# Kernel optimization log

Measured on AMD Instinct MI355X. Metric: run time of the kernel, lower is better.

## Reference

```python
import jax, jax.numpy as jnp
import numpy as np

HEADS = 8

def setup_inputs() -> dict:
    key = jax.random.key(0)
    ks = jax.random.split(key, 6)
    N, C, L = 8, 512, 2048
    s = 0.02
    return {
        'x':  jax.random.normal(ks[0], (N, C, L), dtype=jnp.float32),
        'Wq': jax.random.normal(ks[1], (C, C), dtype=jnp.float32) * s,
        'Wk': jax.random.normal(ks[2], (C, C), dtype=jnp.float32) * s,
        'Wv': jax.random.normal(ks[3], (C, C), dtype=jnp.float32) * s,
        'Wo': jax.random.normal(ks[4], (C, C), dtype=jnp.float32) * s,
        'bo': jnp.zeros((C,), dtype=jnp.float32),
    }

def reference(x, Wq, Wk, Wv, Wo, bo):
    N, C, L = x.shape
    h = HEADS
    d = C // h
    scale = C ** (-0.5)  # note: scales by full channels, as in the original

    def proj(W):
        # Conv1d(k=1, bias=False) == per-position linear: [N,C,L] -> [N,L,h,d]
        y = jnp.einsum('oc,ncl->nlo', W, x)
        return y.reshape(N, L, h, d)

    q, k, v = proj(Wq), proj(Wk), proj(Wv)

    qk = jnp.einsum('nqhd,nkhd->nhqk', q, k)  # [N,h,L,L]
    causal_mask = jnp.tril(jnp.ones((L, L), dtype=bool))
    qk = jnp.where(causal_mask, qk, -jnp.inf)
    attn = jax.nn.softmax(qk * scale, axis=-1)

    out = jnp.einsum('nhqk,nkhd->nqhd', attn, v)  # [N,L,h,d]
    out = out.reshape(N, L, C).transpose(0, 2, 1)  # n (h d) l
    return jnp.einsum('oc,ncl->nol', Wo, out) + bo[None, :, None]
```

## Files before the change

kernel.cpp:

```cpp
#include <hip/hip_runtime.h>
#include <math.h>

typedef __bf16 bf16;
typedef __attribute__((ext_vector_type(8))) __bf16 bf16x8;
typedef __attribute__((ext_vector_type(4))) float f32x4;
typedef unsigned short u16;
typedef unsigned int u32;

constexpr int Nn = 8, Cc = 512, Ll = 2048, Hh = 8, Dd = 64;
constexpr float kScale = 0.044194173824159216f;
constexpr size_t NCL = (size_t)Nn * Cc * Ll;
constexpr size_t WSZ = (size_t)Cc * Cc;

static __device__ __forceinline__ u16 bfbits(bf16 v) {
    union { bf16 b; u16 u; } x; x.b = v; return x.u;
}

#define MFMA(a, b, c) __builtin_amdgcn_mfma_f32_16x16x32_bf16((a), (b), (c), 0, 0, 0)

static __device__ __forceinline__ void async16(const bf16* g, bf16* l) {
    __builtin_amdgcn_global_load_lds(
        (const __attribute__((address_space(1))) void*)g,
        (__attribute__((address_space(3))) void*)l, 16, 0, 0);
}

__global__ __launch_bounds__(256) void xpose_kernel(
    const float* __restrict__ x, bf16* __restrict__ xT)
{
    __shared__ bf16 Ts[64][72];
    const int lt = blockIdx.x, ct = blockIdx.y, n = blockIdx.z;
    const int tid = threadIdx.x;

    const int cr = tid >> 2, l0 = (tid & 3) * 16;
    const float* src = x + ((size_t)(n * Cc + ct * 64 + cr)) * Ll + lt * 64 + l0;
#pragma unroll
    for (int i = 0; i < 4; i++) {
        float4 v = *(const float4*)(src + i * 4);
        Ts[l0 + i * 4 + 0][cr] = (bf16)v.x;
        Ts[l0 + i * 4 + 1][cr] = (bf16)v.y;
        Ts[l0 + i * 4 + 2][cr] = (bf16)v.z;
        Ts[l0 + i * 4 + 3][cr] = (bf16)v.w;
    }
    __syncthreads();

    const int lr = tid >> 2, c0 = (tid & 3) * 16;
    bf16* dst = xT + ((size_t)(n * Ll + lt * 64 + lr)) * Cc + ct * 64 + c0;
    *(bf16x8*)(dst)     = *(const bf16x8*)&Ts[lr][c0];
    *(bf16x8*)(dst + 8) = *(const bf16x8*)&Ts[lr][c0 + 8];
}

__global__ __launch_bounds__(256) void cvtw_kernel(
    const float* __restrict__ Wq, const float* __restrict__ Wk,
    const float* __restrict__ Wv, const float* __restrict__ Wo,
    bf16* __restrict__ Wb)
{
    size_t i = (size_t)blockIdx.x * 256 + threadIdx.x;
    int w = (int)(i >> 16);
    size_t o = i & 65535;
    const float* src = (w == 0) ? Wq : (w == 1) ? Wk : (w == 2) ? Wv : Wo;
    float4 v = ((const float4*)src)[o];
    ushort4 u;
    u.x = bfbits((bf16)v.x); u.y = bfbits((bf16)v.y);
    u.z = bfbits((bf16)v.z); u.w = bfbits((bf16)v.w);
    *(ushort4*)(Wb + (size_t)w * WSZ + o * 4) = u;
}

__global__ __launch_bounds__(256) void qkv_gemm(
    const bf16* __restrict__ xT, const bf16* __restrict__ Wb,
    bf16* __restrict__ Qt, bf16* __restrict__ Kt, bf16* __restrict__ Vb)
{
    const int lt = blockIdx.x, ow = blockIdx.y, n = blockIdx.z;
    const int widx = ow >> 2, otile = ow & 3;

    __shared__ bf16 Xs[128 * 64];
    __shared__ bf16 Ws[128 * 64];

    const int tid = threadIdx.x;
    const int lane = tid & 63, wv = tid >> 6;
    const int m = lane & 15, quad = lane >> 4;
    const int rh = wv & 1, ch = wv >> 1;

    const bf16* __restrict__ W = Wb + (size_t)widx * WSZ + (size_t)otile * 128 * Cc;
    const bf16* __restrict__ X = xT + (size_t)(n * Ll + lt * 128) * Cc;

    int srow[4], scol[4];
#pragma unroll
    for (int i = 0; i < 4; i++) {
        int q = i * 256 + tid;
        srow[i] = q >> 3;
        scol[i] = ((q ^ (q >> 3)) & 7) * 8;
    }

    f32x4 acc[4][4] = {};

    for (int c0 = 0; c0 < Cc; c0 += 64) {
#pragma unroll
        for (int i = 0; i < 4; i++)
            async16(&X[(size_t)srow[i] * Cc + c0 + scol[i]], &Xs[(i * 256 + tid) * 8]);
#pragma unroll
        for (int i = 0; i < 4; i++)
            async16(&W[(size_t)srow[i] * Cc + c0 + scol[i]], &Ws[(i * 256 + tid) * 8]);
        __syncthreads();

        const bf16* TA = (widx < 2) ? Xs : Ws;
        const bf16* TB = (widx < 2) ? Ws : Xs;
#pragma unroll
        for (int kk = 0; kk < 2; kk++) {
            const int sw = (((kk * 4 + quad) ^ (m & 7)) * 8);
            bf16x8 af[4], bfr[4];
#pragma unroll
            for (int t = 0; t < 4; t++)
                af[t] = *(const bf16x8*)&TA[(rh * 64 + t * 16 + m) * 64 + sw];
#pragma unroll
            for (int u = 0; u < 4; u++)
                bfr[u] = *(const bf16x8*)&TB[(ch * 64 + u * 16 + m) * 64 + sw];
#pragma unroll
            for (int t = 0; t < 4; t++)
#pragma unroll
                for (int u = 0; u < 4; u++)
                    acc[t][u] = MFMA(af[t], bfr[u], acc[t][u]);
        }
        __syncthreads();
    }

    if (widx < 2) {
        bf16* __restrict__ OUT = (widx == 0) ? Qt : Kt;
#pragma unroll
        for (int u = 0; u < 4; u++) {
            const int o = otile * 128 + ch * 64 + u * 16 + m;
            const int h = o >> 6, d = o & 63;
            bf16* base = OUT + (size_t)(n * Hh + h) * Ll * Dd + d;
#pragma unroll
            for (int t = 0; t < 4; t++) {
                const int l0 = lt * 128 + rh * 64 + t * 16 + quad * 4;
#pragma unroll
                for (int r = 0; r < 4; r++)
                    base[(size_t)(l0 + r) * Dd] = (bf16)acc[t][u][r];
            }
        }
    } else {
#pragma unroll
        for (int t = 0; t < 4; t++) {
            const int ob = otile * 128 + rh * 64 + t * 16 + quad * 4;
#pragma unroll
            for (int r = 0; r < 4; r++) {
                const int oo = ob + r, h = oo >> 6, d = oo & 63;
                bf16* base = Vb + ((size_t)(n * Hh + h) * Dd + d) * Ll;
#pragma unroll
                for (int u = 0; u < 4; u++)
                    base[lt * 128 + ch * 64 + u * 16 + m] = (bf16)acc[t][u][r];
            }
        }
    }
}

__global__ __launch_bounds__(256) void attn_mfma(
    const bf16* __restrict__ Qt, const bf16* __restrict__ Kt,
    const bf16* __restrict__ Vb, bf16* __restrict__ AO)
{
    const int jp = blockIdx.x;
    const int h  = blockIdx.y, n = blockIdx.z;

    __shared__ bf16 KV[2][2][64 * 72];
    __shared__ bf16 Pbuf[4][32 * 72];

    const int tid = threadIdx.x;
    const int lane = tid & 63, wv = tid >> 6;
    const int m = lane & 15, quad = lane >> 4;

    const size_t bnh = (size_t)(n * Hh + h) * Ll * Dd;
    const bf16* __restrict__ Qh = Qt + bnh;
    const bf16* __restrict__ Kh = Kt + bnh;
    const bf16* __restrict__ Vh = Vb + bnh;

    const int srow = tid >> 3;
    const int sc8  = (tid & 7) * 8;

    bf16* const Pw = &Pbuf[wv][0];

#pragma unroll 1
    for (int ph = 0; ph < 2; ph++) {
        const int st = ph ? (15 - jp) : jp;
        const int R  = st * 128;
        const int nk = 2 * st + 2;
        const int qrow0 = R + wv * 32;

        bf16x8 qf[2][2];
#pragma unroll
        for (int rt = 0; rt < 2; rt++)
#pragma unroll
            for (int hf = 0; hf < 2; hf++)
                qf[rt][hf] = *(const bf16x8*)&Qh[(size_t)(qrow0 + rt * 16 + m) * Dd + hf * 32 + quad * 8];

        f32x4 O[2][4] = {};
        float lsum[2][4] = {{0.f,0.f,0.f,0.f},{0.f,0.f,0.f,0.f}};

        {
            bf16x8 ka  = *(const bf16x8*)&Kh[(size_t)(srow) * Dd + sc8];
            bf16x8 kb2 = *(const bf16x8*)&Kh[(size_t)(srow + 32) * Dd + sc8];
            bf16x8 va  = *(const bf16x8*)&Vh[(size_t)(srow) * Ll + sc8];
            bf16x8 vb2 = *(const bf16x8*)&Vh[(size_t)(srow + 32) * Ll + sc8];
            *(bf16x8*)&KV[0][0][srow * 72 + sc8] = ka;
            *(bf16x8*)&KV[0][0][(srow + 32) * 72 + sc8] = kb2;
            *(bf16x8*)&KV[0][1][srow * 72 + sc8] = va;
            *(bf16x8*)&KV[0][1][(srow + 32) * 72 + sc8] = vb2;
        }
        __syncthreads();

        for (int kt = 0; kt < nk; kt++) {
            const int cur = kt & 1, nxt = cur ^ 1;
            const int kb = kt * 64;
            const bool do_pf = (kt + 1 < nk);

            bf16x8 ka, kb2, va, vb2;
            if (do_pf) {
                const int kn = kb + 64;
                ka  = *(const bf16x8*)&Kh[(size_t)(kn + srow) * Dd + sc8];
                kb2 = *(const bf16x8*)&Kh[(size_t)(kn + srow + 32) * Dd + sc8];
                va  = *(const bf16x8*)&Vh[(size_t)(srow) * Ll + kn + sc8];
                vb2 = *(const bf16x8*)&Vh[(size_t)(srow + 32) * Ll + kn + sc8];
            }

            const bf16* Ks = &KV[cur][0][0];
            const bf16* Vs = &KV[cur][1][0];

            f32x4 S[2][4] = {};
#pragma unroll
            for (int t = 0; t < 4; t++) {
                bf16x8 kf0 = *(const bf16x8*)&Ks[(t * 16 + m) * 72 + quad * 8];
                bf16x8 kf1 = *(const bf16x8*)&Ks[(t * 16 + m) * 72 + 32 + quad * 8];
                S[0][t] = MFMA(qf[0][0], kf0, S[0][t]);
                S[0][t] = MFMA(qf[0][1], kf1, S[0][t]);
                S[1][t] = MFMA(qf[1][0], kf0, S[1][t]);
                S[1][t] = MFMA(qf[1][1], kf1, S[1][t]);
            }

            const bool skip0 = (kb > qrow0 + 15);
            const bool skip1 = (kb > qrow0 + 16 + 15);
#pragma unroll
            for (int rt = 0; rt < 2; rt++) {
                if (rt == 0 ? skip0 : skip1) continue;
                const int qtb = qrow0 + rt * 16;
                const bool dg = (kb + 63 > qtb);
#pragma unroll
                for (int t = 0; t < 4; t++) {
#pragma unroll
                    for (int r = 0; r < 4; r++) {
                        float p = __expf(kScale * S[rt][t][r]);
                        if (dg && (kb + t * 16 + m > qtb + quad * 4 + r)) p = 0.f;
                        lsum[rt][r] += p;
                        Pw[(rt * 16 + quad * 4 + r) * 72 + t * 16 + m] = (bf16)p;
                    }
                }
            }
            asm volatile("s_waitcnt lgkmcnt(0)" ::: "memory");

            bf16x8 pf[2][2];
#pragma unroll
            for (int rt = 0; rt < 2; rt++) {
                if (rt == 0 ? skip0 : skip1) continue;
                pf[rt][0] = *(const bf16x8*)&Pw[(rt * 16 + m) * 72 + quad * 8];
                pf[rt][1] = *(const bf16x8*)&Pw[(rt * 16 + m) * 72 + 32 + quad * 8];
            }
#pragma unroll
            for (int t = 0; t < 4; t++) {
                bf16x8 vf0 = *(const bf16x8*)&Vs[(t * 16 + m) * 72 + quad * 8];
                bf16x8 vf1 = *(const bf16x8*)&Vs[(t * 16 + m) * 72 + 32 + quad * 8];
                if (!skip0) {
                    O[0][t] = MFMA(pf[0][0], vf0, O[0][t]);
                    O[0][t] = MFMA(pf[0][1], vf1, O[0][t]);
                }
                if (!skip1) {
                    O[1][t] = MFMA(pf[1][0], vf0, O[1][t]);
                    O[1][t] = MFMA(pf[1][1], vf1, O[1][t]);
                }
            }

            __syncthreads();
            if (do_pf) {
                *(bf16x8*)&KV[nxt][0][srow * 72 + sc8] = ka;
                *(bf16x8*)&KV[nxt][0][(srow + 32) * 72 + sc8] = kb2;
                *(bf16x8*)&KV[nxt][1][srow * 72 + sc8] = va;
                *(bf16x8*)&KV[nxt][1][(srow + 32) * 72 + sc8] = vb2;
                __syncthreads();
            }
        }

        float inv[2][4];
#pragma unroll
        for (int rt = 0; rt < 2; rt++)
#pragma unroll
            for (int r = 0; r < 4; r++) {
                float s = lsum[rt][r];
#pragma unroll
                for (int off = 1; off < 16; off <<= 1)
                    s += __shfl_xor(s, off, 16);
                inv[rt][r] = 1.0f / s;
            }

        const size_t aobase = (size_t)n * Ll * Cc + (size_t)h * 64;
#pragma unroll
        for (int rt = 0; rt < 2; rt++)
#pragma unroll
            for (int t = 0; t < 4; t++)
#pragma unroll
                for (int r = 0; r < 4; r++) {
                    const int q = qrow0 + rt * 16 + quad * 4 + r;
                    AO[aobase + (size_t)q * Cc + t * 16 + m] =
                        (bf16)(O[rt][t][r] * inv[rt][r]);
                }
    }
}

__global__ __launch_bounds__(256) void out_gemm(
    const bf16* __restrict__ AO, const bf16* __restrict__ Wb,
    const float* __restrict__ bo, float* __restrict__ out)
{
    const int lt = blockIdx.x, ot = blockIdx.y, n = blockIdx.z;

    __shared__ bf16 Ws[128 * 64];
    __shared__ bf16 Bs[128 * 64];

    const int tid = threadIdx.x;
    const int lane = tid & 63, wv = tid >> 6;
    const int m = lane & 15, quad = lane >> 4;
    const int rh = wv & 1, ch = wv >> 1;

    const bf16* __restrict__ W = Wb + 3 * WSZ + (size_t)ot * 128 * Cc;
    const bf16* __restrict__ B = AO + (size_t)(n * Ll + lt * 128) * Cc;

    int srow[4], scol[4];
#pragma unroll
    for (int i = 0; i < 4; i++) {
        int q = i * 256 + tid;
        srow[i] = q >> 3;
        scol[i] = ((q ^ (q >> 3)) & 7) * 8;
    }

    f32x4 acc[4][4] = {};

    for (int c0 = 0; c0 < Cc; c0 += 64) {
#pragma unroll
        for (int i = 0; i < 4; i++)
            async16(&W[(size_t)srow[i] * Cc + c0 + scol[i]], &Ws[(i * 256 + tid) * 8]);
#pragma unroll
        for (int i = 0; i < 4; i++)
            async16(&B[(size_t)srow[i] * Cc + c0 + scol[i]], &Bs[(i * 256 + tid) * 8]);
        __syncthreads();

#pragma unroll
        for (int kk = 0; kk < 2; kk++) {
            const int sw = (((kk * 4 + quad) ^ (m & 7)) * 8);
            bf16x8 af[4], bfr[4];
#pragma unroll
            for (int t = 0; t < 4; t++)
                af[t] = *(const bf16x8*)&Ws[(rh * 64 + t * 16 + m) * 64 + sw];
#pragma unroll
            for (int u = 0; u < 4; u++)
                bfr[u] = *(const bf16x8*)&Bs[(ch * 64 + u * 16 + m) * 64 + sw];
#pragma unroll
            for (int t = 0; t < 4; t++)
#pragma unroll
                for (int u = 0; u < 4; u++)
                    acc[t][u] = MFMA(af[t], bfr[u], acc[t][u]);
        }
        __syncthreads();
    }

#pragma unroll
    for (int t = 0; t < 4; t++) {
        const int ob = ot * 128 + rh * 64 + t * 16 + quad * 4;
#pragma unroll
        for (int r = 0; r < 4; r++) {
            const int o = ob + r;
            const float b = bo[o];
            float* base = out + ((size_t)n * Cc + o) * Ll + lt * 128 + ch * 64;
#pragma unroll
            for (int u = 0; u < 4; u++)
                base[u * 16 + m] = acc[t][u][r] + b;
        }
    }
}

extern "C" void kernel_launch(void* const* d_in, const int* in_sizes, int n_in,
                              void* d_out, int out_size, void* d_ws, size_t ws_size,
                              hipStream_t stream)
{
    const float* x  = (const float*)d_in[0];
    const float* Wq = (const float*)d_in[1];
    const float* Wk = (const float*)d_in[2];
    const float* Wv = (const float*)d_in[3];
    const float* Wo = (const float*)d_in[4];
    const float* bo = (const float*)d_in[5];
    float* out = (float*)d_out;

    bf16* ws = (bf16*)d_ws;
    bf16* xT = ws;
    bf16* Wb = xT + NCL;
    bf16* Qt = Wb + 4 * WSZ;
    bf16* Kt = Qt + NCL;
    bf16* Vb = Kt + NCL;
    bf16* AO = Vb + NCL;

    xpose_kernel<<<dim3(32, 8, Nn), 256, 0, stream>>>(x, xT);
    cvtw_kernel<<<1024, 256, 0, stream>>>(Wq, Wk, Wv, Wo, Wb);
    qkv_gemm<<<dim3(16, 12, Nn), 256, 0, stream>>>(xT, Wb, Qt, Kt, Vb);
    attn_mfma<<<dim3(8, Hh, Nn), 256, 0, stream>>>(Qt, Kt, Vb, AO);
    out_gemm<<<dim3(16, 4, Nn), 256, 0, stream>>>(AO, Wb, bo, out);
}
```

Measured before the change: 233.0 us.

## Fold softmax scale into Q, compute S transposed, and get row sums via MFMA

Pre-multiplies Q by scale·log2(e) in the projection epilogue so the attention inner loop uses a raw exp2 with no multiply. Computes S transposed (K as the A operand) so each lane holds four consecutive keys, which allows packed 8-byte P stores and a per-rt P buffer of half the size. Row sums are accumulated with an MFMA against a ones vector instead of scalar adds and shuffle reductions, and the kernel gets an occupancy hint of 3 blocks. Risks include bf16 truncation of P instead of rounding, an extra LDS wait per row tile, and the row sum now being taken from bf16-rounded P values.

```diff
diff --git a/kernel.cpp b/kernel.cpp
--- a/kernel.cpp
+++ b/kernel.cpp
@@ -9,11 +9,22 @@
 
 constexpr int Nn = 8, Cc = 512, Ll = 2048, Hh = 8, Dd = 64;
 constexpr float kScale = 0.044194173824159216f;
+constexpr float kQexp2 = kScale * 1.44269504088896341f;
 constexpr size_t NCL = (size_t)Nn * Cc * Ll;
 constexpr size_t WSZ = (size_t)Cc * Cc;
 
 static __device__ __forceinline__ u16 bfbits(bf16 v) {
     union { bf16 b; u16 u; } x; x.b = v; return x.u;
+}
+static __device__ __forceinline__ u32 fbits(float f) {
+    union { float f; u32 u; } x; x.f = f; return x.u;
+}
+static __device__ __forceinline__ float fexp2(float x) {
+#if __has_builtin(__builtin_amdgcn_exp2f)
+    return __builtin_amdgcn_exp2f(x);
+#else
+    return exp2f(x);
+#endif
 }
 
 #define MFMA(a, b, c) __builtin_amdgcn_mfma_f32_16x16x32_bf16((a), (b), (c), 0, 0, 0)
@@ -124,6 +135,7 @@
     }
 
     if (widx < 2) {
+        const float fq = (widx == 0) ? kQexp2 : 1.0f;
         bf16* __restrict__ OUT = (widx == 0) ? Qt : Kt;
 #pragma unroll
         for (int u = 0; u < 4; u++) {
@@ -135,7 +147,7 @@
                 const int l0 = lt * 128 + rh * 64 + t * 16 + quad * 4;
 #pragma unroll
                 for (int r = 0; r < 4; r++)
-                    base[(size_t)(l0 + r) * Dd] = (bf16)acc[t][u][r];
+                    base[(size_t)(l0 + r) * Dd] = (bf16)(acc[t][u][r] * fq);
             }
         }
     } else {
@@ -154,7 +166,7 @@
     }
 }
 
-__global__ __launch_bounds__(256) void attn_mfma(
+__global__ __launch_bounds__(256, 3) void attn_mfma(
     const bf16* __restrict__ Qt, const bf16* __restrict__ Kt,
     const bf16* __restrict__ Vb, bf16* __restrict__ AO)
 {
@@ -162,7 +174,7 @@
     const int h  = blockIdx.y, n = blockIdx.z;
 
     __shared__ bf16 KV[2][2][64 * 72];
-    __shared__ bf16 Pbuf[4][32 * 72];
+    __shared__ bf16 Pbuf[4][16 * 72];
 
     const int tid = threadIdx.x;
     const int lane = tid & 63, wv = tid >> 6;
@@ -177,6 +189,14 @@
     const int sc8  = (tid & 7) * 8;
 
     bf16* const Pw = &Pbuf[wv][0];
+
+    bf16x8 ones;
+#pragma unroll
+    for (int j = 0; j < 8; j++) ones[j] = (bf16)1.0f;
+
+    int koff[4];
+#pragma unroll
+    for (int r = 0; r < 4; r++) koff[r] = quad * 4 + r - m;
 
 #pragma unroll 1
     for (int ph = 0; ph < 2; ph++) {
@@ -193,7 +213,7 @@
                 qf[rt][hf] = *(const bf16x8*)&Qh[(size_t)(qrow0 + rt * 16 + m) * Dd + hf * 32 + quad * 8];
 
         f32x4 O[2][4] = {};
-        float lsum[2][4] = {{0.f,0.f,0.f,0.f},{0.f,0.f,0.f,0.f}};
+        f32x4 Ls[2] = {};
 
         {
             bf16x8 ka  = *(const bf16x8*)&Kh[(size_t)(srow) * Dd + sc8];
@@ -224,55 +244,56 @@
             const bf16* Ks = &KV[cur][0][0];
             const bf16* Vs = &KV[cur][1][0];
 
-            f32x4 S[2][4] = {};
+            f32x4 St[2][4] = {};
 #pragma unroll
             for (int t = 0; t < 4; t++) {
                 bf16x8 kf0 = *(const bf16x8*)&Ks[(t * 16 + m) * 72 + quad * 8];
                 bf16x8 kf1 = *(const bf16x8*)&Ks[(t * 16 + m) * 72 + 32 + quad * 8];
-                S[0][t] = MFMA(qf[0][0], kf0, S[0][t]);
-                S[0][t] = MFMA(qf[0][1], kf1, S[0][t]);
-                S[1][t] = MFMA(qf[1][0], kf0, S[1][t]);
-                S[1][t] = MFMA(qf[1][1], kf1, S[1][t]);
+                St[0][t] = MFMA(kf0, qf[0][0], St[0][t]);
+                St[0][t] = MFMA(kf1, qf[0][1], St[0][t]);
+                St[1][t] = MFMA(kf0, qf[1][0], St[1][t]);
+                St[1][t] = MFMA(kf1, qf[1][1], St[1][t]);
             }
 
             const bool skip0 = (kb > qrow0 + 15);
             const bool skip1 = (kb > qrow0 + 16 + 15);
+
 #pragma unroll
             for (int rt = 0; rt < 2; rt++) {
                 if (rt == 0 ? skip0 : skip1) continue;
                 const int qtb = qrow0 + rt * 16;
                 const bool dg = (kb + 63 > qtb);
+                const int thr = qtb - kb;
+
 #pragma unroll
                 for (int t = 0; t < 4; t++) {
-#pragma unroll
-                    for (int r = 0; r < 4; r++) {
-                        float p = __expf(kScale * S[rt][t][r]);
-                        if (dg && (kb + t * 16 + m > qtb + quad * 4 + r)) p = 0.f;
-                        lsum[rt][r] += p;
-                        Pw[(rt * 16 + quad * 4 + r) * 72 + t * 16 + m] = (bf16)p;
+                    float p0 = fexp2(St[rt][t][0]);
+                    float p1 = fexp2(St[rt][t][1]);
+                    float p2 = fexp2(St[rt][t][2]);
+                    float p3 = fexp2(St[rt][t][3]);
+                    if (dg) {
+                        if (t * 16 + koff[0] > thr) p0 = 0.f;
+                        if (t * 16 + koff[1] > thr) p1 = 0.f;
+                        if (t * 16 + koff[2] > thr) p2 = 0.f;
+                        if (t * 16 + koff[3] > thr) p3 = 0.f;
                     }
+                    u32 pk0 = (fbits(p0) >> 16) | (fbits(p1) & 0xFFFF0000u);
+                    u32 pk1 = (fbits(p2) >> 16) | (fbits(p3) & 0xFFFF0000u);
+                    *(uint2*)&Pw[m * 72 + t * 16 + quad * 4] = make_uint2(pk0, pk1);
                 }
-            }
-            asm volatile("s_waitcnt lgkmcnt(0)" ::: "memory");
-
-            bf16x8 pf[2][2];
-#pragma unroll
-            for (int rt = 0; rt < 2; rt++) {
-                if (rt == 0 ? skip0 : skip1) continue;
-                pf[rt][0] = *(const bf16x8*)&Pw[(rt * 16 + m) * 72 + quad * 8];
-                pf[rt][1] = *(const bf16x8*)&Pw[(rt * 16 + m) * 72 + 32 + quad * 8];
-            }
-#pragma unroll
-            for (int t = 0; t < 4; t++) {
-                bf16x8 vf0 = *(const bf16x8*)&Vs[(t * 16 + m) * 72 + quad * 8];
-                bf16x8 vf1 = *(const bf16x8*)&Vs[(t * 16 + m) * 72 + 32 + quad * 8];
-                if (!skip0) {
-                    O[0][t] = MFMA(pf[0][0], vf0, O[0][t]);
-                    O[0][t] = MFMA(pf[0][1], vf1, O[0][t]);
-                }
-                if (!skip1) {
-                    O[1][t] = MFMA(pf[1][0], vf0, O[1][t]);
-                    O[1][t] = MFMA(pf[1][1], vf1, O[1][t]);
+                asm volatile("s_waitcnt lgkmcnt(0)" ::: "memory");
+
+                bf16x8 pf0 = *(const bf16x8*)&Pw[m * 72 + quad * 8];
+                bf16x8 pf1 = *(const bf16x8*)&Pw[m * 72 + 32 + quad * 8];
+
+                Ls[rt] = MFMA(pf0, ones, Ls[rt]);
+                Ls[rt] = MFMA(pf1, ones, Ls[rt]);
+#pragma unroll
+                for (int t = 0; t < 4; t++) {
+                    bf16x8 vf0 = *(const bf16x8*)&Vs[(t * 16 + m) * 72 + quad * 8];
+                    bf16x8 vf1 = *(const bf16x8*)&Vs[(t * 16 + m) * 72 + 32 + quad * 8];
+                    O[rt][t] = MFMA(pf0, vf0, O[rt][t]);
+                    O[rt][t] = MFMA(pf1, vf1, O[rt][t]);
                 }
             }
 
@@ -286,29 +307,21 @@
             }
         }
 
-        float inv[2][4];
-#pragma unroll
-        for (int rt = 0; rt < 2; rt++)
-#pragma unroll
-            for (int r = 0; r < 4; r++) {
-                float s = lsum[rt][r];
-#pragma unroll
-                for (int off = 1; off < 16; off <<= 1)
-                    s += __shfl_xor(s, off, 16);
-                inv[rt][r] = 1.0f / s;
-            }
-
         const size_t aobase = (size_t)n * Ll * Cc + (size_t)h * 64;
 #pragma unroll
-        for (int rt = 0; rt < 2; rt++)
+        for (int rt = 0; rt < 2; rt++) {
+            f32x4 inv;
+#pragma unroll
+            for (int r = 0; r < 4; r++) inv[r] = 1.0f / Ls[rt][r];
 #pragma unroll
             for (int t = 0; t < 4; t++)
 #pragma unroll
                 for (int r = 0; r < 4; r++) {
                     const int q = qrow0 + rt * 16 + quad * 4 + r;
                     AO[aobase + (size_t)q * Cc + t * 16 + m] =
-                        (bf16)(O[rt][t][r] * inv[rt][r]);
+                        (bf16)(O[rt][t][r] * inv[r]);
                 }
+        }
     }
 }
 
```

After: 219.9 us. 1.06x faster.
